# Kernel tuning notes

Measured on AMD Instinct MI355X. Metric: run time of the kernel, lower is better.

Reference implementation:

```python
import jax, jax.numpy as jnp
import numpy as np

B, S, H = 128, 512, 512

def _xavier(key, shape):
    fan_in, fan_out = shape[1], shape[0]
    limit = float(np.sqrt(6.0 / (fan_in + fan_out)))
    return jax.random.uniform(key, shape, jnp.float32, -limit, limit)

def setup_inputs() -> dict:
    key = jax.random.key(0)
    k1, k2, k3, k4, k5 = jax.random.split(key, 5)
    return {
        "h": jax.random.normal(k1, (B, S, H), jnp.float32),
        "x": jax.random.normal(k2, (B, S, H), jnp.float32),
        "Ve": _xavier(k3, (1, H)),
        "U1": _xavier(k4, (H, 2 * H)),
        "U2": _xavier(k5, (H, H)),
    }

def reference(h, x, Ve, U1, U2):
    # h: [B,S,H], x: [B,S,H]
    h_last = h[:, -1, :]                      # [B,H]
    U1a, U1b = U1[:, :U1.shape[0]], U1[:, U1.shape[0]:]  # each [H,H]
    # u1 = concat(h_t, h_last) @ U1.T, vectorized over t
    u1 = jnp.einsum('bsh,kh->bsk', h, U1a) + jnp.einsum('bh,kh->bk', h_last, U1b)[:, None, :]
    u2 = jnp.einsum('bsh,kh->bsk', x, U2)
    u = jnp.tanh(u1 + u2)                     # [B,S,H]
    e = jnp.einsum('bsk,k->bs', u, Ve[0])     # [B,S]
    alpha = jax.nn.softmax(e, axis=1)         # [B,S]
    context = jnp.einsum('bs,bsh->bh', alpha, h)
    return context
```

## Files before the change

kernel.cpp:

```cpp
#include <hip/hip_runtime.h>
#include <cstdint>
#include <cstddef>


typedef _Float16 h8 __attribute__((ext_vector_type(8)));
typedef float    f4 __attribute__((ext_vector_type(4)));

#define GLOAD16(g, l)                                                          \
  __builtin_amdgcn_global_load_lds(                                            \
      (const __attribute__((address_space(1))) void*)(g),                      \
      (__attribute__((address_space(3))) void*)(l), 16, 0, 0)

__device__ __forceinline__ float fast_tanh(float v) {
  float ex = __expf(2.0f * v);
  return 1.0f - 2.0f / (ex + 1.0f);
}

__global__ __launch_bounds__(256)
void cvt2_kernel(const float* __restrict__ h, const float* __restrict__ x,
                 _Float16* __restrict__ hF, _Float16* __restrict__ xF) {
  const int stride = gridDim.x * 256;
  for (int i = blockIdx.x * 256 + threadIdx.x; i < 8388608; i += stride) {
    const bool isH = i < 4194304;
    const float* p = (isH ? h : x) + ((size_t)(i & 4194303)) * 8;
    _Float16* d = (isH ? hF : xF) + ((size_t)(i & 4194303)) * 8;
    f4 a = *(const f4*)p, b = *(const f4*)(p + 4);
    _Float16 hv[8];
    hv[0]=(_Float16)a[0]; hv[1]=(_Float16)a[1]; hv[2]=(_Float16)a[2]; hv[3]=(_Float16)a[3];
    hv[4]=(_Float16)b[0]; hv[5]=(_Float16)b[1]; hv[6]=(_Float16)b[2]; hv[7]=(_Float16)b[3];
    *(uint4*)d = *(uint4*)hv;
  }
}

__global__ void bsetup4_kernel(const float* __restrict__ U1, const float* __restrict__ U2,
                               _Float16* __restrict__ Bimg) {
  int g = blockIdx.x * 256 + threadIdx.x;
  int c   = g & 2047;
  int kt  = (g >> 11) & 15;
  int nt  = g >> 15;
  int l15 = c & 15;
  int lhi = (c >> 4) & 3;
  int kk  = (c >> 6) & 1;
  int nf  = (c >> 7) & 3;
  int wn  = c >> 9;
  int n = nt * 256 + wn * 64 + nf * 16 + l15;
  int k = kt * 64 + kk * 32 + lhi * 8;
  const float* p = (k < 512) ? (U1 + (size_t)n * 1024 + k)
                             : (U2 + (size_t)n * 512 + (k - 512));
  f4 a = *(const f4*)p, b = *(const f4*)(p + 4);
  _Float16 hv[8];
  hv[0]=(_Float16)a[0]; hv[1]=(_Float16)a[1]; hv[2]=(_Float16)a[2]; hv[3]=(_Float16)a[3];
  hv[4]=(_Float16)b[0]; hv[5]=(_Float16)b[1]; hv[6]=(_Float16)b[2]; hv[7]=(_Float16)b[3];
  *(uint4*)(Bimg + (size_t)g * 8) = *(uint4*)hv;
}

__global__ __launch_bounds__(256)
void bias2_kernel(const float* __restrict__ hT, const float* __restrict__ U1,
                  float* __restrict__ bias) {
  const int t = threadIdx.x, l = t & 63, w = t >> 6;
  const int n = blockIdx.x * 4 + w;
  const float4* ur = (const float4*)(U1 + (size_t)n * 1024 + 512);
  const float4 u0 = ur[l], u1 = ur[l + 64];
#pragma unroll 4
  for (int b = 0; b < 128; ++b) {
    const float4* hp = (const float4*)(hT + ((size_t)b * 512 + 511) * 512);
    float4 h0 = hp[l], h1 = hp[l + 64];
    float s = u0.x*h0.x + u0.y*h0.y + u0.z*h0.z + u0.w*h0.w
            + u1.x*h1.x + u1.y*h1.y + u1.z*h1.z + u1.w*h1.w;
#pragma unroll
    for (int d = 1; d < 64; d <<= 1) s += __shfl_xor(s, d, 64);
    if (l == 0) bias[(size_t)b * 512 + n] = s;
  }
}

__global__ __launch_bounds__(512, 2)
void gemm5_kernel(const _Float16* __restrict__ hF, const _Float16* __restrict__ xF,
                  const _Float16* __restrict__ Bimg, const float* __restrict__ bias,
                  const float* __restrict__ Ve, float* __restrict__ e) {
  const int bid  = ((int)blockIdx.x & 7) * 128 + ((int)blockIdx.x >> 3);
  const int bm   = bid >> 1;
  const int nt   = bid & 1;
  const int row0 = bm * 128;
  const int bb   = row0 >> 9;
  const int t    = threadIdx.x;
  const int l    = t & 63;
  const int wv   = t >> 6;
  const int wm   = wv >> 2, wn = wv & 3;
  const int l15  = l & 15, lhi = l >> 4;

  __shared__ __align__(16) _Float16 Asm[3][8192];
  __shared__ __align__(16) _Float16 Bsm[3][16384];

  const int aoff0 = (wv * 16 + (l >> 3)) * 512 + (((l & 7) ^ (l >> 3)) << 3);

  auto STAGE = [&](int buf, int kt) {
    const _Float16* ah = ((kt < 8) ? hF : xF) + (size_t)row0 * 512 + (kt & 7) * 64;
    _Float16* Ad = &Asm[buf][wv * 1024];
    GLOAD16(ah + aoff0,        Ad);
    GLOAD16(ah + aoff0 + 4096, Ad + 512);
    const _Float16* bt = Bimg + ((size_t)(nt * 16 + kt) << 14);
    _Float16* Bd = &Bsm[buf][wv * 512];
#pragma unroll
    for (int j = 0; j < 4; ++j)
      GLOAD16(bt + j * 4096 + wv * 512 + l * 8, Bd + j * 4096);
  };

  const int aBase = (wm * 64 + l15) * 64;
  const int b2  = (l15 >> 2) & 1;
  const int lo2 = lhi ^ (l15 & 3);
  const int ak0 = ((((0 ^ b2) << 2) | lo2) << 3);
  const int ak1 = ((((1 ^ b2) << 2) | lo2) << 3);
  const int bBase = wn * 4096 + l * 8;

  f4 acc[4][4];
#pragma unroll
  for (int mf = 0; mf < 4; ++mf)
#pragma unroll
    for (int nf = 0; nf < 4; ++nf)
      acc[mf][nf] = (f4){0.f, 0.f, 0.f, 0.f};

  STAGE(0, 0);
  STAGE(1, 1);
  asm volatile("s_waitcnt vmcnt(6)\n\ts_barrier" ::: "memory");
  __builtin_amdgcn_sched_barrier(0);

  int bc = 0;
  for (int kt = 0; kt < 16; ++kt) {
    if (kt < 14) {
      int bp = bc + 2; if (bp >= 3) bp -= 3;
      STAGE(bp, kt + 2);
    }
    const _Float16* Ab = &Asm[bc][0];
    const _Float16* Bb = &Bsm[bc][0];
#pragma unroll
    for (int kk = 0; kk < 2; ++kk) {
      h8 af[4], bf[4];
      const int akk = kk ? ak1 : ak0;
#pragma unroll
      for (int mf = 0; mf < 4; ++mf)
        af[mf] = *(const h8*)&Ab[aBase + mf * 1024 + akk];
#pragma unroll
      for (int nf = 0; nf < 4; ++nf)
        bf[nf] = *(const h8*)&Bb[bBase + nf * 1024 + kk * 512];
      __builtin_amdgcn_s_setprio(1);
#pragma unroll
      for (int mf = 0; mf < 4; ++mf)
#pragma unroll
        for (int nf = 0; nf < 4; ++nf)
          acc[mf][nf] = __builtin_amdgcn_mfma_f32_16x16x32_f16(af[mf], bf[nf], acc[mf][nf], 0, 0, 0);
      __builtin_amdgcn_s_setprio(0);
    }
    if (kt < 14) {
      asm volatile("s_waitcnt vmcnt(6)\n\ts_barrier" ::: "memory");
      __builtin_amdgcn_sched_barrier(0);
    } else if (kt == 14) {
      asm volatile("s_waitcnt vmcnt(0)\n\ts_barrier" ::: "memory");
      __builtin_amdgcn_sched_barrier(0);
    }
    bc = bc + 1; if (bc == 3) bc = 0;
  }

  float vev[4], biasv[4];
#pragma unroll
  for (int nf = 0; nf < 4; ++nf) {
    int c = nt * 256 + wn * 64 + nf * 16 + l15;
    vev[nf]   = Ve[c];
    biasv[nf] = bias[(size_t)bb * 512 + c];
  }
#pragma unroll
  for (int mf = 0; mf < 4; ++mf) {
#pragma unroll
    for (int j = 0; j < 4; ++j) {
      float s = 0.f;
#pragma unroll
      for (int nf = 0; nf < 4; ++nf)
        s += fast_tanh(acc[mf][nf][j] + biasv[nf]) * vev[nf];
#pragma unroll
      for (int m = 1; m < 16; m <<= 1) s += __shfl_xor(s, m, 64);
      if (l15 == 0) atomicAdd(&e[row0 + wm * 64 + mf * 16 + lhi * 4 + j], s);
    }
  }
}

__global__ __launch_bounds__(512)
void smax_ctx_kernel(const _Float16* __restrict__ hF, const float* __restrict__ e,
                     float* __restrict__ out) {
  const int b  = blockIdx.x >> 2;
  const int sc = blockIdx.x & 3;
  const int t  = threadIdx.x;
  __shared__ float al[512];
  __shared__ float redm[8], reds[8];
  float v = e[(size_t)b * 512 + t];
  float m = v;
#pragma unroll
  for (int d = 1; d < 64; d <<= 1) m = fmaxf(m, __shfl_xor(m, d, 64));
  if ((t & 63) == 0) redm[t >> 6] = m;
  __syncthreads();
  m = redm[0];
#pragma unroll
  for (int i = 1; i < 8; ++i) m = fmaxf(m, redm[i]);
  float ev = __expf(v - m);
  al[t] = ev;
  float s = ev;
#pragma unroll
  for (int d = 1; d < 64; d <<= 1) s += __shfl_xor(s, d, 64);
  if ((t & 63) == 0) reds[t >> 6] = s;
  __syncthreads();
  s = reds[0];
#pragma unroll
  for (int i = 1; i < 8; ++i) s += reds[i];
  const float inv = 1.0f / s;
  const _Float16* hp = hF + ((size_t)b * 512 + sc * 128) * 512 + t;
  float acc = 0.f;
#pragma unroll 4
  for (int q = 0; q < 128; ++q) acc += al[sc * 128 + q] * (float)hp[(size_t)q * 512];
  atomicAdd(&out[(size_t)b * 512 + t], acc * inv);
}

extern "C" void kernel_launch(void* const* d_in, const int* in_sizes, int n_in,
                              void* d_out, int out_size, void* d_ws, size_t ws_size,
                              hipStream_t stream) {
  const float* h  = (const float*)d_in[0];
  const float* x  = (const float*)d_in[1];
  const float* Ve = (const float*)d_in[2];
  const float* U1 = (const float*)d_in[3];
  const float* U2 = (const float*)d_in[4];
  float* out = (float*)d_out;

  const size_t MB = 1u << 20;
  if (ws_size < 130 * MB) return;

  _Float16* hF   = (_Float16*)d_ws;
  _Float16* xF   = (_Float16*)((char*)d_ws + 64 * MB);
  _Float16* Bimg = (_Float16*)((char*)d_ws + 128 * MB);
  float*    bias = (float*)((char*)d_ws + 129 * MB);
  float*    e    = (float*)((char*)d_ws + 129 * MB + 256 * 1024);

  hipMemsetAsync(e, 0, 65536 * sizeof(float), stream);
  hipMemsetAsync(d_out, 0, 65536 * sizeof(float), stream);

  cvt2_kernel<<<4096, 256, 0, stream>>>(h, x, hF, xF);
  bsetup4_kernel<<<256, 256, 0, stream>>>(U1, U2, Bimg);
  bias2_kernel<<<128, 256, 0, stream>>>(h, U1, bias);
  gemm5_kernel<<<1024, 512, 0, stream>>>(hF, xF, Bimg, bias, Ve, e);
  smax_ctx_kernel<<<512, 512, 0, stream>>>(hF, e, out);
}
```

Before: 272.9 us.

## Shrink GEMM tile to 128x128, load B fragments directly into registers

Changes the fused GEMM from 512-thread blocks computing 128x256 tiles to 256-thread blocks computing 128x128 tiles, doubling the grid. The B operand is no longer staged through LDS: each wave loads its pre-swizzled fragments straight from global memory into registers, double-buffered across even and odd k-steps. A is double-buffered in LDS instead of triple-buffered, and the B image layout is regenerated to match. The goal is less LDS traffic and footprint and higher occupancy, at the cost of re-reading A from global memory twice as often and more register pressure.

```diff
diff --git a/kernel.cpp b/kernel.cpp
--- a/kernel.cpp
+++ b/kernel.cpp
@@ -10,6 +10,14 @@
   __builtin_amdgcn_global_load_lds(                                            \
       (const __attribute__((address_space(1))) void*)(g),                      \
       (__attribute__((address_space(3))) void*)(l), 16, 0, 0)
+
+#define SB() __builtin_amdgcn_sched_barrier(0)
+
+#define PBAR(N)                                                                \
+  do {                                                                         \
+    asm volatile("s_waitcnt vmcnt(" #N ") lgkmcnt(0)\n\ts_barrier" ::: "memory"); \
+    SB();                                                                      \
+  } while (0)
 
 __device__ __forceinline__ float fast_tanh(float v) {
   float ex = __expf(2.0f * v);
@@ -32,18 +40,17 @@
   }
 }
 
-__global__ void bsetup4_kernel(const float* __restrict__ U1, const float* __restrict__ U2,
+__global__ void bsetup5_kernel(const float* __restrict__ U1, const float* __restrict__ U2,
                                _Float16* __restrict__ Bimg) {
   int g = blockIdx.x * 256 + threadIdx.x;
-  int c   = g & 2047;
-  int kt  = (g >> 11) & 15;
-  int nt  = g >> 15;
-  int l15 = c & 15;
-  int lhi = (c >> 4) & 3;
-  int kk  = (c >> 6) & 1;
-  int nf  = (c >> 7) & 3;
-  int wn  = c >> 9;
-  int n = nt * 256 + wn * 64 + nf * 16 + l15;
+  int l15 = g & 15;
+  int lhi = (g >> 4) & 3;
+  int kk  = (g >> 6) & 1;
+  int nf  = (g >> 7) & 3;
+  int wn  = (g >> 9) & 1;
+  int kt  = (g >> 10) & 15;
+  int nt  = g >> 14;
+  int n = nt * 128 + wn * 64 + nf * 16 + l15;
   int k = kt * 64 + kk * 32 + lhi * 8;
   const float* p = (k < 512) ? (U1 + (size_t)n * 1024 + k)
                              : (U2 + (size_t)n * 512 + (k - 512));
@@ -73,36 +80,39 @@
   }
 }
 
-__global__ __launch_bounds__(512, 2)
-void gemm5_kernel(const _Float16* __restrict__ hF, const _Float16* __restrict__ xF,
+__global__ __launch_bounds__(256, 2)
+void gemm6_kernel(const _Float16* __restrict__ hF, const _Float16* __restrict__ xF,
                   const _Float16* __restrict__ Bimg, const float* __restrict__ bias,
                   const float* __restrict__ Ve, float* __restrict__ e) {
-  const int bid  = ((int)blockIdx.x & 7) * 128 + ((int)blockIdx.x >> 3);
-  const int bm   = bid >> 1;
-  const int nt   = bid & 1;
+  const int bid  = ((int)blockIdx.x & 7) * 256 + ((int)blockIdx.x >> 3);
+  const int bm   = bid >> 2;
+  const int nt   = bid & 3;
   const int row0 = bm * 128;
   const int bb   = row0 >> 9;
   const int t    = threadIdx.x;
   const int l    = t & 63;
   const int wv   = t >> 6;
-  const int wm   = wv >> 2, wn = wv & 3;
+  const int wm   = wv >> 1, wn = wv & 1;
   const int l15  = l & 15, lhi = l >> 4;
 
-  __shared__ __align__(16) _Float16 Asm[3][8192];
-  __shared__ __align__(16) _Float16 Bsm[3][16384];
-
-  const int aoff0 = (wv * 16 + (l >> 3)) * 512 + (((l & 7) ^ (l >> 3)) << 3);
-
-  auto STAGE = [&](int buf, int kt) {
+  __shared__ __align__(16) _Float16 Asm[2][8192];
+
+  const int aoff0 = (wv * 32 + (l >> 3)) * 512 + (((l & 7) ^ (l >> 3)) << 3);
+
+  auto STAGEA = [&](int c, int kt) {
     const _Float16* ah = ((kt < 8) ? hF : xF) + (size_t)row0 * 512 + (kt & 7) * 64;
-    _Float16* Ad = &Asm[buf][wv * 1024];
-    GLOAD16(ah + aoff0,        Ad);
-    GLOAD16(ah + aoff0 + 4096, Ad + 512);
-    const _Float16* bt = Bimg + ((size_t)(nt * 16 + kt) << 14);
-    _Float16* Bd = &Bsm[buf][wv * 512];
 #pragma unroll
     for (int j = 0; j < 4; ++j)
-      GLOAD16(bt + j * 4096 + wv * 512 + l * 8, Bd + j * 4096);
+      GLOAD16(ah + aoff0 + j * 4096, &Asm[c][wv * 2048 + j * 512]);
+  };
+
+  h8 bE[8], bO[8];
+  auto LOADB = [&](h8* b, int kt) {
+    const _Float16* bt = Bimg + ((size_t)(nt * 16 + kt) << 13)
+                              + (size_t)(wn * 512 + l) * 8;
+#pragma unroll
+    for (int i = 0; i < 8; ++i)
+      b[i] = *(const h8*)(bt + ((i & 3) * 128 + (i >> 2) * 64) * 8);
   };
 
   const int aBase = (wm * 64 + l15) * 64;
@@ -110,7 +120,6 @@
   const int lo2 = lhi ^ (l15 & 3);
   const int ak0 = ((((0 ^ b2) << 2) | lo2) << 3);
   const int ak1 = ((((1 ^ b2) << 2) | lo2) << 3);
-  const int bBase = wn * 4096 + l * 8;
 
   f4 acc[4][4];
 #pragma unroll
@@ -119,51 +128,44 @@
     for (int nf = 0; nf < 4; ++nf)
       acc[mf][nf] = (f4){0.f, 0.f, 0.f, 0.f};
 
-  STAGE(0, 0);
-  STAGE(1, 1);
-  asm volatile("s_waitcnt vmcnt(6)\n\ts_barrier" ::: "memory");
-  __builtin_amdgcn_sched_barrier(0);
-
-  int bc = 0;
-  for (int kt = 0; kt < 16; ++kt) {
-    if (kt < 14) {
-      int bp = bc + 2; if (bp >= 3) bp -= 3;
-      STAGE(bp, kt + 2);
-    }
-    const _Float16* Ab = &Asm[bc][0];
-    const _Float16* Bb = &Bsm[bc][0];
+  auto COMPUTE = [&](const _Float16* Ab, const h8* b) {
 #pragma unroll
     for (int kk = 0; kk < 2; ++kk) {
-      h8 af[4], bf[4];
       const int akk = kk ? ak1 : ak0;
+      h8 af[4];
 #pragma unroll
       for (int mf = 0; mf < 4; ++mf)
         af[mf] = *(const h8*)&Ab[aBase + mf * 1024 + akk];
 #pragma unroll
-      for (int nf = 0; nf < 4; ++nf)
-        bf[nf] = *(const h8*)&Bb[bBase + nf * 1024 + kk * 512];
-      __builtin_amdgcn_s_setprio(1);
-#pragma unroll
       for (int mf = 0; mf < 4; ++mf)
 #pragma unroll
         for (int nf = 0; nf < 4; ++nf)
-          acc[mf][nf] = __builtin_amdgcn_mfma_f32_16x16x32_f16(af[mf], bf[nf], acc[mf][nf], 0, 0, 0);
-      __builtin_amdgcn_s_setprio(0);
+          acc[mf][nf] = __builtin_amdgcn_mfma_f32_16x16x32_f16(af[mf], b[kk * 4 + nf], acc[mf][nf], 0, 0, 0);
     }
-    if (kt < 14) {
-      asm volatile("s_waitcnt vmcnt(6)\n\ts_barrier" ::: "memory");
-      __builtin_amdgcn_sched_barrier(0);
-    } else if (kt == 14) {
-      asm volatile("s_waitcnt vmcnt(0)\n\ts_barrier" ::: "memory");
-      __builtin_amdgcn_sched_barrier(0);
+  };
+
+  STAGEA(0, 0); SB();
+  LOADB(bE, 0); SB();
+  PBAR(4);
+
+  for (int kp = 0; kp < 8; ++kp) {
+    const int kt0 = kp * 2;
+    STAGEA(1, kt0 + 1); SB();
+    LOADB(bO, kt0 + 1); SB();
+    COMPUTE(&Asm[0][0], bE);
+    PBAR(4);
+    if (kp < 7) {
+      STAGEA(0, kt0 + 2); SB();
+      LOADB(bE, kt0 + 2); SB();
     }
-    bc = bc + 1; if (bc == 3) bc = 0;
+    COMPUTE(&Asm[1][0], bO);
+    if (kp < 7) PBAR(4);
   }
 
   float vev[4], biasv[4];
 #pragma unroll
   for (int nf = 0; nf < 4; ++nf) {
-    int c = nt * 256 + wn * 64 + nf * 16 + l15;
+    int c = nt * 128 + wn * 64 + nf * 16 + l15;
     vev[nf]   = Ve[c];
     biasv[nf] = bias[(size_t)bb * 512 + c];
   }
@@ -240,8 +242,8 @@
   hipMemsetAsync(d_out, 0, 65536 * sizeof(float), stream);
 
   cvt2_kernel<<<4096, 256, 0, stream>>>(h, x, hF, xF);
-  bsetup4_kernel<<<256, 256, 0, stream>>>(U1, U2, Bimg);
+  bsetup5_kernel<<<256, 256, 0, stream>>>(U1, U2, Bimg);
   bias2_kernel<<<128, 256, 0, stream>>>(h, U1, bias);
-  gemm5_kernel<<<1024, 512, 0, stream>>>(hF, xF, Bimg, bias, Ve, e);
+  gemm6_kernel<<<2048, 256, 0, stream>>>(hF, xF, Bimg, bias, Ve, e);
   smax_ctx_kernel<<<512, 512, 0, stream>>>(hF, e, out);
 }
```

Result: faster. 251.4 us (-7.9%).
